# Performance work log

Measured on AMD Instinct MI355X. Metric: run time of the kernel, lower is better.

Reference implementation:

```python
import jax, jax.numpy as jnp
import numpy as np

B, M, N, L = 4096, 100, 80, 10


def setup_inputs() -> dict:
    key = jax.random.key(0)
    k1, k2, k3, k4 = jax.random.split(key, 4)
    x_ini = jax.random.normal(k1, (B, N, 1), dtype=jnp.float32)
    y = jax.random.normal(k2, (B, M, 1), dtype=jnp.float32)
    H = jax.random.normal(k3, (B, M, N), dtype=jnp.float32)
    xt = jax.random.normal(k4, (B, N, 1), dtype=jnp.float32)
    # learned per-iteration scalars, initialized exactly as in __init__
    ILbar = jnp.full((L,), 1.0 / 250.0, dtype=jnp.float32)
    tau = jnp.full((L,), 250.0, dtype=jnp.float32)
    ramp = 0.48 - (0.48 - 0.001) / L * jnp.arange(L, dtype=jnp.float32)
    gamma1 = ramp
    gamma3 = ramp
    return {"x_ini": x_ini, "y": y, "H": H, "xt": xt,
            "ILbar": ILbar, "tau": tau, "gamma1": gamma1, "gamma3": gamma3}


def reference(x_ini, y, H, xt, ILbar, tau, gamma1, gamma3):
    n = x_ini.shape[1]
    x = x_ini
    z = x_ini
    u = jnp.zeros_like(x_ini)
    Ht = jnp.swapaxes(H, 1, 2)              # [B, N, M]
    HTH = jnp.matmul(Ht, H)                 # [B, N, N]
    HTy = jnp.matmul(Ht, y)                 # [B, N, 1]
    eye = jnp.eye(n, dtype=H.dtype)
    for ii in range(ILbar.shape[0]):
        A = HTH + tau[ii] * eye             # [B, N, N]
        rhs = HTy + u + tau[ii] * z         # [B, N, 1]
        x = jnp.linalg.solve(A, rhs)        # == inv(A) @ rhs
        t = x - u * ILbar[ii]
        z = (jnp.tanh(t * (0.5 / gamma1[ii]))
             + jnp.tanh((t - 2.0) * (0.5 / gamma3[ii]))
             + jnp.tanh((t + 2.0) * (0.5 / gamma3[ii])))
        u = u + tau[ii] * (z - x)
    dx = x - xt
    dz = z - xt
    # sum_b (dx^T dx) + sum_b (dz^T dz)  -> shape [1, 1]
    loss = (jnp.sum(dx * dx) + jnp.sum(dz * dz)).reshape(1, 1)
    return x, loss
```

## Files before the change

kernel.cpp:

```cpp
#include <hip/hip_runtime.h>

#define NB 4096
#define MD 100
#define ND 80
#define LI 10
#define NIT 10
#define MT 10
#define WPB 4

#define WAVE_SYNC() asm volatile("s_waitcnt lgkmcnt(0)" ::: "memory")

__global__ void zero_loss_k(float* out) {
    if (threadIdx.x == 0) out[(size_t)NB * ND] = 0.f;
}

__device__ __forceinline__ float fast_tanh(float a) {
    float e = __builtin_amdgcn_exp2f(a * 2.885390082f);
    return 1.f - 2.f * __builtin_amdgcn_rcpf(e + 1.f);
}

__global__ __launch_bounds__(64 * WPB, 1) void admm_k(
    const float* __restrict__ x_ini, const float* __restrict__ y,
    const float* __restrict__ H,     const float* __restrict__ xt,
    const float* __restrict__ ILb,   const float* __restrict__ tauA,
    const float* __restrict__ g1A,   const float* __restrict__ g3A,
    float* __restrict__ out)
{
    __shared__ __align__(16) float Hs[WPB][MT * ND];
    __shared__ __align__(16) float ys[WPB][MD + 4];
    __shared__ __align__(16) float xb[WPB][2][ND];

    const int w  = threadIdx.x >> 6;
    const int l  = threadIdx.x & 63;
    const int b  = blockIdx.x * WPB + w;
    const int r0 = l >> 2;
    const int s4 = l & 3;

    if (l < MD / 4)
        ((float4*)ys[w])[l] = ((const float4*)(y + (size_t)b * MD))[l];

    float A[5][20];
    float hty[5];
    #pragma unroll
    for (int g = 0; g < 5; ++g) {
        hty[g] = 0.f;
        #pragma unroll
        for (int c = 0; c < 20; ++c) A[g][c] = 0.f;
    }

    const float* Hg = H + (size_t)b * (MD * ND);
    for (int t = 0; t < MD / MT; ++t) {
        WAVE_SYNC();
        {
            const float4* src = (const float4*)(Hg + t * MT * ND);
            float4* dst = (float4*)Hs[w];
            float4 v0 = src[l], v1 = src[64 + l], v2 = src[128 + l];
            dst[l] = v0; dst[64 + l] = v1; dst[128 + l] = v2;
            if (l < 8) dst[192 + l] = src[192 + l];
        }
        WAVE_SYNC();
        #pragma unroll
        for (int mm = 0; mm < MT; ++mm) {
            const float yv = ys[w][t * MT + mm];
            float cv[5];
            #pragma unroll
            for (int g = 0; g < 5; ++g) cv[g] = Hs[w][mm * ND + r0 + 16 * g];
            #pragma unroll
            for (int j = 0; j < 5; ++j) {
                const float4 rv = *(const float4*)&Hs[w][mm * ND + s4 * 20 + 4 * j];
                #pragma unroll
                for (int g = 0; g < 5; ++g) {
                    A[g][4 * j + 0] = fmaf(cv[g], rv.x, A[g][4 * j + 0]);
                    A[g][4 * j + 1] = fmaf(cv[g], rv.y, A[g][4 * j + 1]);
                    A[g][4 * j + 2] = fmaf(cv[g], rv.z, A[g][4 * j + 2]);
                    A[g][4 * j + 3] = fmaf(cv[g], rv.w, A[g][4 * j + 3]);
                }
            }
            #pragma unroll
            for (int g = 0; g < 5; ++g) hty[g] = fmaf(cv[g], yv, hty[g]);
        }
    }

    float mx;
    {
        float rs[5];
        #pragma unroll
        for (int g = 0; g < 5; ++g) {
            float s = 0.f;
            #pragma unroll
            for (int c = 0; c < 20; ++c) s += fabsf(A[g][c]);
            rs[g] = s;
        }
        #pragma unroll
        for (int g = 0; g < 5; ++g) {
            rs[g] += __shfl_xor(rs[g], 1);
            rs[g] += __shfl_xor(rs[g], 2);
        }
        mx = rs[0];
        #pragma unroll
        for (int g = 1; g < 5; ++g) mx = fmaxf(mx, rs[g]);
        #pragma unroll
        for (int off = 4; off < 64; off <<= 1) mx = fmaxf(mx, __shfl_xor(mx, off));
    }
    const float lam = mx;

    float xr[5], zr[5], ur[5];
    #pragma unroll
    for (int g = 0; g < 5; ++g) {
        const float v = x_ini[(size_t)b * ND + r0 + 16 * g];
        xr[g] = v; zr[g] = v; ur[g] = 0.f;
    }

    int par = 0;
    auto matvec = [&](float (&acc)[5]) {
        const float* xp = &xb[w][par][0];
        {
            const float4 v = *(const float4*)&xp[s4 * 20];
            #pragma unroll
            for (int g = 0; g < 5; ++g)
                acc[g] = fmaf(A[g][3], v.w, fmaf(A[g][2], v.z,
                         fmaf(A[g][1], v.y, A[g][0] * v.x)));
        }
        #pragma unroll
        for (int j = 1; j < 5; ++j) {
            const float4 v = *(const float4*)&xp[s4 * 20 + 4 * j];
            #pragma unroll
            for (int g = 0; g < 5; ++g) {
                acc[g] = fmaf(A[g][4 * j + 0], v.x, acc[g]);
                acc[g] = fmaf(A[g][4 * j + 1], v.y, acc[g]);
                acc[g] = fmaf(A[g][4 * j + 2], v.z, acc[g]);
                acc[g] = fmaf(A[g][4 * j + 3], v.w, acc[g]);
            }
        }
        #pragma unroll
        for (int g = 0; g < 5; ++g) {
            acc[g] += __shfl_xor(acc[g], 1);
            acc[g] += __shfl_xor(acc[g], 2);
        }
    };

    for (int ii = 0; ii < LI; ++ii) {
        const float tau = tauA[ii];
        const float ilb = ILb[ii];
        const float g1s = 0.5f / g1A[ii];
        const float g3s = 0.5f / g3A[ii];
        const float delta = 0.5f * lam;
        const float theta = tau + delta;
        const float sigma = theta / delta;
        const float invth = 1.f / theta;
        const float twod  = 2.f / delta;

        float rres[5], dk[5], acc[5];

        if (s4 == 0) {
            #pragma unroll
            for (int g = 0; g < 5; ++g) xb[w][par][r0 + 16 * g] = xr[g];
        }
        WAVE_SYNC();
        matvec(acc);
        #pragma unroll
        for (int g = 0; g < 5; ++g) {
            rres[g] = (hty[g] + ur[g] + tau * zr[g]) - (acc[g] + tau * xr[g]);
            dk[g] = rres[g] * invth;
        }
        par ^= 1;
        float rho = delta / theta;

        for (int k = 1; k < NIT; ++k) {
            #pragma unroll
            for (int g = 0; g < 5; ++g) xr[g] += dk[g];
            if (s4 == 0) {
                #pragma unroll
                for (int g = 0; g < 5; ++g) xb[w][par][r0 + 16 * g] = dk[g];
            }
            WAVE_SYNC();
            matvec(acc);
            #pragma unroll
            for (int g = 0; g < 5; ++g) rres[g] -= acc[g] + tau * dk[g];
            const float rhon = 1.f / (2.f * sigma - rho);
            #pragma unroll
            for (int g = 0; g < 5; ++g) dk[g] = rhon * (rho * dk[g] + twod * rres[g]);
            rho = rhon;
            par ^= 1;
        }
        #pragma unroll
        for (int g = 0; g < 5; ++g) xr[g] += dk[g];

        #pragma unroll
        for (int g = 0; g < 5; ++g) {
            const float tt = xr[g] - ur[g] * ilb;
            zr[g] = fast_tanh(tt * g1s) + fast_tanh((tt - 2.f) * g3s)
                  + fast_tanh((tt + 2.f) * g3s);
            ur[g] = fmaf(tau, zr[g] - xr[g], ur[g]);
        }
    }

    float lv = 0.f;
    #pragma unroll
    for (int g = 0; g < 5; ++g) {
        const float xtr = xt[(size_t)b * ND + r0 + 16 * g];
        const float dx = xr[g] - xtr, dz = zr[g] - xtr;
        lv += dx * dx + dz * dz;
        if (s4 == 0) out[(size_t)b * ND + r0 + 16 * g] = xr[g];
    }
    if (s4 != 0) lv = 0.f;
    #pragma unroll
    for (int off = 1; off < 64; off <<= 1) lv += __shfl_xor(lv, off);
    if (l == 0) atomicAdd(out + (size_t)NB * ND, lv);
}

extern "C" void kernel_launch(void* const* d_in, const int* in_sizes, int n_in,
                              void* d_out, int out_size, void* d_ws, size_t ws_size,
                              hipStream_t stream) {
    const float* x_ini = (const float*)d_in[0];
    const float* y     = (const float*)d_in[1];
    const float* H     = (const float*)d_in[2];
    const float* xt    = (const float*)d_in[3];
    const float* ILb   = (const float*)d_in[4];
    const float* tauA  = (const float*)d_in[5];
    const float* g1A   = (const float*)d_in[6];
    const float* g3A   = (const float*)d_in[7];
    float* out = (float*)d_out;

    zero_loss_k<<<1, 64, 0, stream>>>(out);
    admm_k<<<NB / WPB, 64 * WPB, 0, stream>>>(x_ini, y, H, xt, ILb, tauA, g1A, g3A, out);
}
```

Before: 369.2 us.

## Replace LDS vector staging in matvec with ds_bpermute cross-lane gathers

The matvec no longer writes the iterate vector to shared memory and waits on the LDS counter before reading it back. Each lane now pulls the vector elements it needs straight from the owning lanes with ds_bpermute. To make that gather pattern work, the per-lane column layout of the register-resident A changes from contiguous (s4*20+i) to strided (s4+4i). As a consequence, the HᵀH build now does 20 scalar LDS loads per row instead of 5 float4 loads. The intent is to shorten the dependent store/sync/load chain inside the serial inner solver, at the cost of more LDS instructions during the Gram-matrix build.

```diff
diff --git a/kernel.cpp b/kernel.cpp
--- a/kernel.cpp
+++ b/kernel.cpp
@@ -17,6 +17,10 @@
 __device__ __forceinline__ float fast_tanh(float a) {
     float e = __builtin_amdgcn_exp2f(a * 2.885390082f);
     return 1.f - 2.f * __builtin_amdgcn_rcpf(e + 1.f);
+}
+
+__device__ __forceinline__ float bperm(int byte_addr, float v) {
+    return __int_as_float(__builtin_amdgcn_ds_bpermute(byte_addr, __float_as_int(v)));
 }
 
 __global__ __launch_bounds__(64 * WPB, 1) void admm_k(
@@ -28,13 +32,16 @@
 {
     __shared__ __align__(16) float Hs[WPB][MT * ND];
     __shared__ __align__(16) float ys[WPB][MD + 4];
-    __shared__ __align__(16) float xb[WPB][2][ND];
 
     const int w  = threadIdx.x >> 6;
     const int l  = threadIdx.x & 63;
     const int b  = blockIdx.x * WPB + w;
     const int r0 = l >> 2;
     const int s4 = l & 3;
+
+    int addr[4];
+    #pragma unroll
+    for (int k = 0; k < 4; ++k) addr[k] = (s4 + 4 * k) << 4;
 
     if (l < MD / 4)
         ((float4*)ys[w])[l] = ((const float4*)(y + (size_t)b * MD))[l];
@@ -66,15 +73,11 @@
             #pragma unroll
             for (int g = 0; g < 5; ++g) cv[g] = Hs[w][mm * ND + r0 + 16 * g];
             #pragma unroll
-            for (int j = 0; j < 5; ++j) {
-                const float4 rv = *(const float4*)&Hs[w][mm * ND + s4 * 20 + 4 * j];
+            for (int i = 0; i < 20; ++i) {
+                const float rv = Hs[w][mm * ND + s4 + 4 * i];
                 #pragma unroll
-                for (int g = 0; g < 5; ++g) {
-                    A[g][4 * j + 0] = fmaf(cv[g], rv.x, A[g][4 * j + 0]);
-                    A[g][4 * j + 1] = fmaf(cv[g], rv.y, A[g][4 * j + 1]);
-                    A[g][4 * j + 2] = fmaf(cv[g], rv.z, A[g][4 * j + 2]);
-                    A[g][4 * j + 3] = fmaf(cv[g], rv.w, A[g][4 * j + 3]);
-                }
+                for (int g = 0; g < 5; ++g)
+                    A[g][i] = fmaf(cv[g], rv, A[g][i]);
             }
             #pragma unroll
             for (int g = 0; g < 5; ++g) hty[g] = fmaf(cv[g], yv, hty[g]);
@@ -111,25 +114,21 @@
         xr[g] = v; zr[g] = v; ur[g] = 0.f;
     }
 
-    int par = 0;
-    auto matvec = [&](float (&acc)[5]) {
-        const float* xp = &xb[w][par][0];
-        {
-            const float4 v = *(const float4*)&xp[s4 * 20];
-            #pragma unroll
-            for (int g = 0; g < 5; ++g)
-                acc[g] = fmaf(A[g][3], v.w, fmaf(A[g][2], v.z,
-                         fmaf(A[g][1], v.y, A[g][0] * v.x)));
-        }
-        #pragma unroll
-        for (int j = 1; j < 5; ++j) {
-            const float4 v = *(const float4*)&xp[s4 * 20 + 4 * j];
+    auto matvec = [&](const float (&src)[5], float (&acc)[5]) {
+        #pragma unroll
+        for (int g = 0; g < 5; ++g) acc[g] = 0.f;
+        #pragma unroll
+        for (int gs = 0; gs < 5; ++gs) {
+            const float x0 = bperm(addr[0], src[gs]);
+            const float x1 = bperm(addr[1], src[gs]);
+            const float x2 = bperm(addr[2], src[gs]);
+            const float x3 = bperm(addr[3], src[gs]);
             #pragma unroll
             for (int g = 0; g < 5; ++g) {
-                acc[g] = fmaf(A[g][4 * j + 0], v.x, acc[g]);
-                acc[g] = fmaf(A[g][4 * j + 1], v.y, acc[g]);
-                acc[g] = fmaf(A[g][4 * j + 2], v.z, acc[g]);
-                acc[g] = fmaf(A[g][4 * j + 3], v.w, acc[g]);
+                acc[g] = fmaf(A[g][4 * gs + 0], x0, acc[g]);
+                acc[g] = fmaf(A[g][4 * gs + 1], x1, acc[g]);
+                acc[g] = fmaf(A[g][4 * gs + 2], x2, acc[g]);
+                acc[g] = fmaf(A[g][4 * gs + 3], x3, acc[g]);
             }
         }
         #pragma unroll
@@ -152,36 +151,24 @@
 
         float rres[5], dk[5], acc[5];
 
-        if (s4 == 0) {
-            #pragma unroll
-            for (int g = 0; g < 5; ++g) xb[w][par][r0 + 16 * g] = xr[g];
-        }
-        WAVE_SYNC();
-        matvec(acc);
+        matvec(xr, acc);
         #pragma unroll
         for (int g = 0; g < 5; ++g) {
             rres[g] = (hty[g] + ur[g] + tau * zr[g]) - (acc[g] + tau * xr[g]);
             dk[g] = rres[g] * invth;
         }
-        par ^= 1;
         float rho = delta / theta;
 
         for (int k = 1; k < NIT; ++k) {
             #pragma unroll
             for (int g = 0; g < 5; ++g) xr[g] += dk[g];
-            if (s4 == 0) {
-                #pragma unroll
-                for (int g = 0; g < 5; ++g) xb[w][par][r0 + 16 * g] = dk[g];
-            }
-            WAVE_SYNC();
-            matvec(acc);
+            matvec(dk, acc);
             #pragma unroll
             for (int g = 0; g < 5; ++g) rres[g] -= acc[g] + tau * dk[g];
             const float rhon = 1.f / (2.f * sigma - rho);
             #pragma unroll
             for (int g = 0; g < 5; ++g) dk[g] = rhon * (rho * dk[g] + twod * rres[g]);
             rho = rhon;
-            par ^= 1;
         }
         #pragma unroll
         for (int g = 0; g < 5; ++g) xr[g] += dk[g];
```

New measurement: 530.2 us. +43.6%, slower.
